# Optimization experiments

Measured on AMD Instinct MI355X. Metric: run time of the kernel, lower is better.

## Reference

```python
import jax, jax.numpy as jnp
import numpy as np

N, E, T = 10000, 160000, 1600000
D, C, H = 256, 64, 1024  # d_model, d_message/channels, 4*d_model ffn hidden


def setup_inputs() -> dict:
    key = jax.random.key(0)
    ks = jax.random.split(key, 20)
    rn = lambda k, s, sc=1.0: jax.random.normal(k, s, dtype=jnp.float32) * sc
    return {
        "x": rn(ks[0], (N, D)),
        "y": rn(ks[1], (E, D)),
        "r": rn(ks[2], (E, 3)),
        "src": jax.random.randint(ks[3], (E,), 0, N),
        "dst": jax.random.randint(ks[4], (E,), 0, N),
        "tsrc": jax.random.randint(ks[5], (T,), 0, E),
        "tdst": jax.random.randint(ks[6], (T,), 0, E),
        "W_src": rn(ks[7], (D, C), 0.05), "b_src": rn(ks[8], (C,), 0.05),
        "W_dst": rn(ks[9], (D, C), 0.05), "b_dst": rn(ks[10], (C,), 0.05),
        "W_edge": rn(ks[11], (D, C), 0.05), "b_edge": rn(ks[12], (C,), 0.05),
        "attn": rn(ks[13], (C,), 0.05),
        "W1": rn(ks[14], (C, H), 0.05), "b1": rn(ks[15], (H,), 0.05),
        "W2": rn(ks[16], (H, D), 0.05), "b2": rn(ks[17], (D,), 0.05),
    }


def reference(x, y, r, src, dst, tsrc, tdst,
              W_src, b_src, W_dst, b_dst, W_edge, b_edge,
              attn, W1, b1, W2, b2):
    # per-bond message: xij = Lin_src(x)[src] + Lin_dst(x)[dst] + Lin_edge(y)  -> (E, C)
    xij = (x @ W_src + b_src)[src] + (x @ W_dst + b_dst)[dst] + (y @ W_edge + b_edge)

    # triplet angle cosine via normalized (negated) bond vectors  -> (T,)
    rnorm = -r / jnp.linalg.norm(r, axis=1, keepdims=True)
    cos_jik = jnp.clip(jnp.sum(rnorm[tsrc] * rnorm[tdst], axis=-1), -1.0 + 1e-6, 1.0 - 1e-6)

    # Chebyshev expansion: T_n(cos) = cos(n * arccos(cos))  -> (T, C)
    n = jnp.arange(C, dtype=jnp.float32)
    z_jik = jnp.cos(n[None, :] * jnp.arccos(cos_jik)[:, None])

    # triplet feature and attention logit
    e_jik = jax.nn.silu(z_jik + xij[tsrc] + xij[tdst])          # (T, C)
    logits = e_jik @ attn                                        # (T,)

    # segment softmax over triplets grouped by destination bond (edge_softmax)
    mx = jax.ops.segment_max(logits, tdst, num_segments=E)
    ex = jnp.exp(logits - mx[tdst])
    den = jax.ops.segment_sum(ex, tdst, num_segments=E)
    a = ex / den[tdst]                                           # (T,)

    # attention-weighted scatter-sum of neighbor bond features  -> (E, C)
    ft = jax.ops.segment_sum(xij[tsrc] * a[:, None], tdst, num_segments=E)

    # feedforward: Linear -> SiLU -> Linear  -> (E, D)
    return jax.nn.silu(ft @ W1 + b1) @ W2 + b2
```

## Files before the change

kernel.cpp:

```cpp
#include <hip/hip_runtime.h>

#define N_NODES 10000
#define N_EDGES 160000
#define N_TRI   1600000
#define DM      256
#define CH      64
#define HH      1024

typedef short bf16x8 __attribute__((ext_vector_type(8)));
typedef float f32x4  __attribute__((ext_vector_type(4)));

__device__ __forceinline__ unsigned short f2bf(float f) {
  unsigned int u = __float_as_uint(f);
  u += 0x7fff + ((u >> 16) & 1);
  return (unsigned short)(u >> 16);
}

__global__ __launch_bounds__(256) void k_node_proj(
    const float* __restrict__ x, const float* __restrict__ Ws, const float* __restrict__ bs,
    const float* __restrict__ Wd, const float* __restrict__ bd,
    float* __restrict__ xs, float* __restrict__ xd) {
  __shared__ float xl[4][DM];
  int tid = threadIdx.x;
  int n0 = blockIdx.x * 4;
  for (int i = tid; i < 4 * DM; i += 256) xl[i >> 8][i & 255] = x[n0 * DM + i];
  __syncthreads();
  int c = tid & 63, g = tid >> 6;
  float as = bs[c], ad = bd[c];
  for (int d = 0; d < DM; d++) {
    float xv = xl[g][d];
    as += xv * Ws[d * CH + c];
    ad += xv * Wd[d * CH + c];
  }
  int n = n0 + g;
  xs[n * CH + c] = as;
  xd[n * CH + c] = ad;
}

__global__ __launch_bounds__(256) void k_edge_proj(
    const float* __restrict__ y, const float* __restrict__ We, const float* __restrict__ be,
    const float* __restrict__ xs, const float* __restrict__ xd,
    const int* __restrict__ src, const int* __restrict__ dst,
    float* __restrict__ xij) {
  __shared__ float yl[16][DM];
  int tid = threadIdx.x;
  int e0 = blockIdx.x * 16;
  for (int i = tid; i < 16 * DM; i += 256) yl[i >> 8][i & 255] = y[e0 * DM + i];
  __syncthreads();
  int c = tid & 63, g = tid >> 6;
  float acc[4];
#pragma unroll
  for (int s = 0; s < 4; s++) acc[s] = be[c];
  for (int d = 0; d < DM; d += 4) {
    float w0 = We[(d + 0) * CH + c];
    float w1 = We[(d + 1) * CH + c];
    float w2 = We[(d + 2) * CH + c];
    float w3 = We[(d + 3) * CH + c];
#pragma unroll
    for (int s = 0; s < 4; s++) {
      const float4 yv = *(const float4*)&yl[g * 4 + s][d];
      acc[s] += yv.x * w0 + yv.y * w1 + yv.z * w2 + yv.w * w3;
    }
  }
#pragma unroll
  for (int s = 0; s < 4; s++) {
    int e = e0 + g * 4 + s;
    xij[e * CH + c] = acc[s] + xs[src[e] * CH + c] + xd[dst[e] * CH + c];
  }
}

__global__ void k_rnorm(const float* __restrict__ r, float4* __restrict__ rn4) {
  int e = blockIdx.x * 256 + threadIdx.x;
  if (e >= N_EDGES) return;
  float a = r[e * 3 + 0], b = r[e * 3 + 1], c = r[e * 3 + 2];
  float inv = rsqrtf(a * a + b * b + c * c);
  rn4[e] = (float4){-a * inv, -b * inv, -c * inv, 0.f};
}

__global__ __launch_bounds__(256) void k_theta(
    const float4* __restrict__ rn4, const int* __restrict__ tsrc, const int* __restrict__ tdst,
    float* __restrict__ theta) {
  int t = blockIdx.x * 256 + threadIdx.x;
  if (t >= N_TRI) return;
  float4 a = rn4[tsrc[t]];
  float4 b = rn4[tdst[t]];
  float c = a.x * b.x + a.y * b.y + a.z * b.z;
  c = fminf(fmaxf(c, -1.0f + 1e-6f), 1.0f - 1e-6f);
  theta[t] = acosf(c);
}

__global__ void k_hist(const int* __restrict__ tdst, int* __restrict__ cnt) {
  int t = blockIdx.x * 256 + threadIdx.x;
  if (t < N_TRI) atomicAdd(&cnt[tdst[t]], 1);
}

__global__ __launch_bounds__(256) void k_scan_sum(const int* __restrict__ cnt,
                                                  int* __restrict__ bsum, int n) {
  __shared__ int s[256];
  int b = blockIdx.x, tid = threadIdx.x;
  int tot = 0;
#pragma unroll
  for (int i = 0; i < 8; i++) {
    int idx = b * 2048 + i * 256 + tid;
    if (idx < n) tot += cnt[idx];
  }
  s[tid] = tot;
  __syncthreads();
  for (int off = 128; off > 0; off >>= 1) {
    if (tid < off) s[tid] += s[tid + off];
    __syncthreads();
  }
  if (tid == 0) bsum[b] = s[0];
}

__global__ void k_scan_top(int* __restrict__ bsum, int nb, int* __restrict__ start_last) {
  if (threadIdx.x == 0) {
    int run = 0;
    for (int i = 0; i < nb; i++) {
      int v = bsum[i];
      bsum[i] = run;
      run += v;
    }
    *start_last = run;
  }
}

__global__ __launch_bounds__(256) void k_scan_apply(const int* __restrict__ cnt,
                                                    const int* __restrict__ bsum,
                                                    int* __restrict__ start,
                                                    int* __restrict__ cur, int n) {
  __shared__ int s[256];
  int b = blockIdx.x, tid = threadIdx.x;
  int base = b * 2048 + tid * 8;
  int loc[8];
  int tot = 0;
#pragma unroll
  for (int i = 0; i < 8; i++) {
    int idx = base + i;
    int v = (idx < n) ? cnt[idx] : 0;
    loc[i] = tot;
    tot += v;
  }
  s[tid] = tot;
  __syncthreads();
  for (int off = 1; off < 256; off <<= 1) {
    int t2 = 0;
    if (tid >= off) t2 = s[tid - off];
    __syncthreads();
    if (tid >= off) s[tid] += t2;
    __syncthreads();
  }
  int excl = s[tid] - tot + bsum[b];
#pragma unroll
  for (int i = 0; i < 8; i++) {
    int idx = base + i;
    if (idx < n) {
      int v = excl + loc[i];
      start[idx] = v;
      cur[idx] = v;
    }
  }
}

__global__ void k_scatter(const int* __restrict__ tdst, int* __restrict__ cur,
                          int* __restrict__ sorted) {
  int t = blockIdx.x * 256 + threadIdx.x;
  if (t < N_TRI) {
    int p = atomicAdd(&cur[tdst[t]], 1);
    sorted[p] = t;
  }
}

__global__ __launch_bounds__(256) void k_attn_ft(
    const int* __restrict__ start, const int* __restrict__ sorted,
    const float* __restrict__ theta, const int* __restrict__ tsrc,
    const float* __restrict__ xij, const float* __restrict__ attn,
    unsigned short* __restrict__ ft) {
  int tid = threadIdx.x;
  int e = blockIdx.x * 4 + (tid >> 6);
  int lane = tid & 63;
  float lanef = (float)lane;
  int beg = start[e], end = start[e + 1];
  int deg = end - beg;
  float xd = xij[e * CH + lane];
  float av = attn[lane];
  float m = -1e30f, den = 0.f, acc = 0.f;
  if (deg > 0 && deg <= 64) {
    int ts_ = 0;
    float th_ = 0.f;
    if (lane < deg) {
      int t = sorted[beg + lane];
      ts_ = tsrc[t];
      th_ = theta[t];
    }
    int ts_cur = __shfl(ts_, 0);
    float th_cur = __shfl(th_, 0);
    float xs_cur = xij[ts_cur * CH + lane];
    for (int i = 0; i < deg; i++) {
      float th_nxt = 0.f, xs_nxt = 0.f;
      if (i + 1 < deg) {
        int ts_nxt = __shfl(ts_, i + 1);
        th_nxt = __shfl(th_, i + 1);
        xs_nxt = xij[ts_nxt * CH + lane];
      }
      float v = __cosf(th_cur * lanef) + xs_cur + xd;
      float sv = v / (1.f + __expf(-v));
      float contrib = sv * av;
#pragma unroll
      for (int off = 32; off; off >>= 1) contrib += __shfl_xor(contrib, off);
      float mn = fmaxf(m, contrib);
      float scale = __expf(m - mn);
      float p = __expf(contrib - mn);
      den = den * scale + p;
      acc = acc * scale + p * xs_cur;
      m = mn;
      th_cur = th_nxt;
      xs_cur = xs_nxt;
    }
  } else if (deg > 64) {
    for (int i = 0; i < deg; i++) {
      int t = sorted[beg + i];
      int ts = tsrc[t];
      float th = theta[t];
      float xs = xij[ts * CH + lane];
      float v = __cosf(th * lanef) + xs + xd;
      float sv = v / (1.f + __expf(-v));
      float contrib = sv * av;
#pragma unroll
      for (int off = 32; off; off >>= 1) contrib += __shfl_xor(contrib, off);
      float mn = fmaxf(m, contrib);
      float scale = __expf(m - mn);
      float p = __expf(contrib - mn);
      den = den * scale + p;
      acc = acc * scale + p * xs;
      m = mn;
    }
  }
  ft[e * CH + lane] = f2bf(deg > 0 ? acc / den : 0.f);
}

__global__ __launch_bounds__(256) void k_prep_w1p(const float* __restrict__ W1,
                                                  unsigned short* __restrict__ W1P) {
  int idx = blockIdx.x * 256 + threadIdx.x;
  int k = idx & 63, row = idx >> 6;
  int i = row & 15, t = (row >> 4) & 1, hb = row >> 5;
  int hidden = hb * 32 + ((i >> 2) << 3) + (t << 2) + (i & 3);
  W1P[idx] = f2bf(W1[k * HH + hidden]);
}

__global__ __launch_bounds__(256) void k_prep_w2t(const float* __restrict__ W2,
                                                  unsigned short* __restrict__ W2T) {
  int idx = blockIdx.x * 256 + threadIdx.x;
  int n = idx >> 10, k = idx & 1023;
  W2T[idx] = f2bf(W2[k * DM + n]);
}

__global__ __launch_bounds__(256, 3) void k_ffn_mfma3(
    const unsigned short* __restrict__ ft, const unsigned short* __restrict__ W1P,
    const float* __restrict__ b1, const unsigned short* __restrict__ W2T,
    const float* __restrict__ b2, float* __restrict__ out) {
  __shared__ __align__(16) unsigned short hbuf[2][4 * 64 * 8];
  int tid = threadIdx.x;
  int w = tid >> 6, lane = tid & 63;
  int l16 = lane & 15, q = lane >> 4;
  int e0 = blockIdx.x * 64;

  bf16x8 ftf[2];
#pragma unroll
  for (int s = 0; s < 2; s++)
    ftf[s] = *(const bf16x8*)&ft[(size_t)(e0 + w * 16 + l16) * CH + s * 32 + q * 8];

  f32x4 acc[4][4];
#pragma unroll
  for (int mt = 0; mt < 4; mt++)
#pragma unroll
    for (int nt = 0; nt < 4; nt++) acc[mt][nt] = (f32x4){0.f, 0.f, 0.f, 0.f};

  bf16x8 w1f[2][2];
#pragma unroll
  for (int t = 0; t < 2; t++)
#pragma unroll
    for (int s = 0; s < 2; s++)
      w1f[t][s] = *(const bf16x8*)&W1P[(size_t)(t * 16 + l16) * 64 + s * 32 + q * 8];

  int p = 0;
  for (int hb = 0; hb < 32; hb++) {
    bf16x8 bw[4];
#pragma unroll
    for (int nt = 0; nt < 4; nt++)
      bw[nt] = *(const bf16x8*)&W2T[(size_t)(w * 64 + nt * 16 + l16) * HH + hb * 32 + q * 8];

    f32x4 h0 = (f32x4){0.f, 0.f, 0.f, 0.f};
    f32x4 h1 = (f32x4){0.f, 0.f, 0.f, 0.f};
    h0 = __builtin_amdgcn_mfma_f32_16x16x32_bf16(w1f[0][0], ftf[0], h0, 0, 0, 0);
    h0 = __builtin_amdgcn_mfma_f32_16x16x32_bf16(w1f[0][1], ftf[1], h0, 0, 0, 0);
    h1 = __builtin_amdgcn_mfma_f32_16x16x32_bf16(w1f[1][0], ftf[0], h1, 0, 0, 0);
    h1 = __builtin_amdgcn_mfma_f32_16x16x32_bf16(w1f[1][1], ftf[1], h1, 0, 0, 0);

    const float4 bv0 = *(const float4*)&b1[hb * 32 + q * 8];
    const float4 bv1 = *(const float4*)&b1[hb * 32 + q * 8 + 4];
    float v0 = h0[0] + bv0.x, v1 = h0[1] + bv0.y, v2 = h0[2] + bv0.z, v3 = h0[3] + bv0.w;
    float w0 = h1[0] + bv1.x, w1_ = h1[1] + bv1.y, w2 = h1[2] + bv1.z, w3 = h1[3] + bv1.w;
    float s0 = v0 / (1.f + __expf(-v0)), s1 = v1 / (1.f + __expf(-v1));
    float s2 = v2 / (1.f + __expf(-v2)), s3 = v3 / (1.f + __expf(-v3));
    float t0 = w0 / (1.f + __expf(-w0)), t1 = w1_ / (1.f + __expf(-w1_));
    float t2 = w2 / (1.f + __expf(-w2)), t3 = w3 / (1.f + __expf(-w3));
    union { bf16x8 v; unsigned int u[4]; } pa;
    pa.u[0] = ((unsigned int)f2bf(s1) << 16) | f2bf(s0);
    pa.u[1] = ((unsigned int)f2bf(s3) << 16) | f2bf(s2);
    pa.u[2] = ((unsigned int)f2bf(t1) << 16) | f2bf(t0);
    pa.u[3] = ((unsigned int)f2bf(t3) << 16) | f2bf(t2);
    *(bf16x8*)&hbuf[p][(w * 64 + lane) * 8] = pa.v;

    int hbn = (hb < 31) ? hb + 1 : 31;
    bf16x8 w1n[2][2];
#pragma unroll
    for (int t = 0; t < 2; t++)
#pragma unroll
      for (int s = 0; s < 2; s++)
        w1n[t][s] = *(const bf16x8*)&W1P[(size_t)((hbn * 2 + t) * 16 + l16) * 64 + s * 32 + q * 8];

    __syncthreads();

    bf16x8 pam[4];
#pragma unroll
    for (int mt = 0; mt < 4; mt++)
      pam[mt] = *(const bf16x8*)&hbuf[p][(mt * 64 + lane) * 8];
#pragma unroll
    for (int nt = 0; nt < 4; nt++)
#pragma unroll
      for (int mt = 0; mt < 4; mt++)
        acc[mt][nt] = __builtin_amdgcn_mfma_f32_16x16x32_bf16(pam[mt], bw[nt], acc[mt][nt], 0, 0, 0);

#pragma unroll
    for (int t = 0; t < 2; t++)
#pragma unroll
      for (int s = 0; s < 2; s++) w1f[t][s] = w1n[t][s];
    p ^= 1;
  }

#pragma unroll
  for (int nt = 0; nt < 4; nt++) {
    int col = w * 64 + nt * 16 + l16;
    float b2v = b2[col];
#pragma unroll
    for (int mt = 0; mt < 4; mt++) {
      int erow = e0 + mt * 16 + q * 4;
#pragma unroll
      for (int r = 0; r < 4; r++)
        out[(size_t)(erow + r) * DM + col] = acc[mt][nt][r] + b2v;
    }
  }
}

extern "C" void kernel_launch(void* const* d_in, const int* in_sizes, int n_in,
                              void* d_out, int out_size, void* d_ws, size_t ws_size,
                              hipStream_t stream) {
  (void)in_sizes; (void)n_in; (void)out_size; (void)ws_size;
  const float* x      = (const float*)d_in[0];
  const float* y      = (const float*)d_in[1];
  const float* r      = (const float*)d_in[2];
  const int*   src    = (const int*)d_in[3];
  const int*   dst    = (const int*)d_in[4];
  const int*   tsrc   = (const int*)d_in[5];
  const int*   tdst   = (const int*)d_in[6];
  const float* W_src  = (const float*)d_in[7];
  const float* b_src  = (const float*)d_in[8];
  const float* W_dst  = (const float*)d_in[9];
  const float* b_dst  = (const float*)d_in[10];
  const float* W_edge = (const float*)d_in[11];
  const float* b_edge = (const float*)d_in[12];
  const float* attn   = (const float*)d_in[13];
  const float* W1     = (const float*)d_in[14];
  const float* b1     = (const float*)d_in[15];
  const float* W2     = (const float*)d_in[16];
  const float* b2     = (const float*)d_in[17];
  float* out = (float*)d_out;

  char* wsp = (char*)d_ws;
  auto alloc = [&](size_t bytes) -> char* {
    char* p = wsp;
    wsp += (bytes + 255) & ~(size_t)255;
    return p;
  };
  float* xs     = (float*)alloc((size_t)N_NODES * CH * 4);
  float* xd     = (float*)alloc((size_t)N_NODES * CH * 4);
  float* xij    = (float*)alloc((size_t)N_EDGES * CH * 4);
  float4* rn4   = (float4*)alloc((size_t)N_EDGES * 16);
  float* theta  = (float*)alloc((size_t)N_TRI * 4);
  int*   cnt    = (int*)alloc((size_t)N_EDGES * 4);
  int*   start  = (int*)alloc((size_t)(N_EDGES + 1) * 4);
  int*   cur    = (int*)alloc((size_t)N_EDGES * 4);
  int*   bsum   = (int*)alloc(1024 * 4);
  int*   sorted = (int*)alloc((size_t)N_TRI * 4);
  unsigned short* ftb = (unsigned short*)alloc((size_t)N_EDGES * CH * 2);
  unsigned short* W1P = (unsigned short*)alloc((size_t)CH * HH * 2);
  unsigned short* W2T = (unsigned short*)alloc((size_t)HH * DM * 2);

  const int NB = (N_EDGES + 2047) / 2048;

  k_prep_w1p<<<(CH * HH) / 256, 256, 0, stream>>>(W1, W1P);
  k_prep_w2t<<<(HH * DM) / 256, 256, 0, stream>>>(W2, W2T);

  k_node_proj<<<N_NODES / 4, 256, 0, stream>>>(x, W_src, b_src, W_dst, b_dst, xs, xd);
  k_rnorm<<<N_EDGES / 256, 256, 0, stream>>>(r, rn4);
  k_edge_proj<<<N_EDGES / 16, 256, 0, stream>>>(y, W_edge, b_edge, xs, xd, src, dst, xij);
  k_theta<<<N_TRI / 256, 256, 0, stream>>>(rn4, tsrc, tdst, theta);

  hipMemsetAsync(cnt, 0, (size_t)N_EDGES * 4, stream);
  k_hist<<<N_TRI / 256, 256, 0, stream>>>(tdst, cnt);
  k_scan_sum<<<NB, 256, 0, stream>>>(cnt, bsum, N_EDGES);
  k_scan_top<<<1, 64, 0, stream>>>(bsum, NB, &start[N_EDGES]);
  k_scan_apply<<<NB, 256, 0, stream>>>(cnt, bsum, start, cur, N_EDGES);
  k_scatter<<<N_TRI / 256, 256, 0, stream>>>(tdst, cur, sorted);

  k_attn_ft<<<N_EDGES / 4, 256, 0, stream>>>(start, sorted, theta, tsrc, xij, attn, ftb);
  k_ffn_mfma3<<<N_EDGES / 64, 256, 0, stream>>>(ftb, W1P, b1, W2T, b2, out);
}
```

Baseline: 1.228 ms.

## Use two-pass lane-parallel softmax and remove LDS exchange in FFN kernel

In the attention kernel, degrees up to 64 now take a two-pass path. The first pass collects each triplet's logit into one lane, then a wave reduction computes the max and denominator. A second pass reloads neighbour features and accumulates the attention-weighted sum, replacing the per-step online-softmax rescaling with its serial exps. In the FFN kernel, each wave now computes the hidden activations for all four row tiles itself and feeds them straight into the second MFMA, removing the shared-memory buffer and block barrier. The cost is redundant first-layer MFMA work, more registers and lower launch-bound occupancy, plus a second gather of xij in attention.

```diff
diff --git a/kernel.cpp b/kernel.cpp
--- a/kernel.cpp
+++ b/kernel.cpp
@@ -184,7 +184,7 @@
   int deg = end - beg;
   float xd = xij[e * CH + lane];
   float av = attn[lane];
-  float m = -1e30f, den = 0.f, acc = 0.f;
+  float acc = 0.f;
   if (deg > 0 && deg <= 64) {
     int ts_ = 0;
     float th_ = 0.f;
@@ -193,6 +193,7 @@
       ts_ = tsrc[t];
       th_ = theta[t];
     }
+    float l_mine = -1e30f;
     int ts_cur = __shfl(ts_, 0);
     float th_cur = __shfl(th_, 0);
     float xs_cur = xij[ts_cur * CH + lane];
@@ -208,16 +209,31 @@
       float contrib = sv * av;
 #pragma unroll
       for (int off = 32; off; off >>= 1) contrib += __shfl_xor(contrib, off);
-      float mn = fmaxf(m, contrib);
-      float scale = __expf(m - mn);
-      float p = __expf(contrib - mn);
-      den = den * scale + p;
-      acc = acc * scale + p * xs_cur;
-      m = mn;
+      if (lane == i) l_mine = contrib;
       th_cur = th_nxt;
       xs_cur = xs_nxt;
     }
+    float mx = l_mine;
+#pragma unroll
+    for (int off = 32; off; off >>= 1) mx = fmaxf(mx, __shfl_xor(mx, off));
+    float ex = (lane < deg) ? __expf(l_mine - mx) : 0.f;
+    float den = ex;
+#pragma unroll
+    for (int off = 32; off; off >>= 1) den += __shfl_xor(den, off);
+    float a_mine = ex / den;
+    ts_cur = __shfl(ts_, 0);
+    xs_cur = xij[ts_cur * CH + lane];
+    for (int i = 0; i < deg; i++) {
+      float xs_nxt = 0.f;
+      if (i + 1 < deg) {
+        int ts_nxt = __shfl(ts_, i + 1);
+        xs_nxt = xij[ts_nxt * CH + lane];
+      }
+      acc += __shfl(a_mine, i) * xs_cur;
+      xs_cur = xs_nxt;
+    }
   } else if (deg > 64) {
+    float m = -1e30f, den = 0.f;
     for (int i = 0; i < deg; i++) {
       int t = sorted[beg + i];
       int ts = tsrc[t];
@@ -235,8 +251,9 @@
       acc = acc * scale + p * xs;
       m = mn;
     }
-  }
-  ft[e * CH + lane] = f2bf(deg > 0 ? acc / den : 0.f);
+    acc = acc / den;
+  }
+  ft[e * CH + lane] = f2bf(acc);
 }
 
 __global__ __launch_bounds__(256) void k_prep_w1p(const float* __restrict__ W1,
@@ -255,20 +272,21 @@
   W2T[idx] = f2bf(W2[k * DM + n]);
 }
 
-__global__ __launch_bounds__(256, 3) void k_ffn_mfma3(
+__global__ __launch_bounds__(256, 2) void k_ffn_mfma4(
     const unsigned short* __restrict__ ft, const unsigned short* __restrict__ W1P,
     const float* __restrict__ b1, const unsigned short* __restrict__ W2T,
     const float* __restrict__ b2, float* __restrict__ out) {
-  __shared__ __align__(16) unsigned short hbuf[2][4 * 64 * 8];
   int tid = threadIdx.x;
   int w = tid >> 6, lane = tid & 63;
   int l16 = lane & 15, q = lane >> 4;
   int e0 = blockIdx.x * 64;
 
-  bf16x8 ftf[2];
-#pragma unroll
-  for (int s = 0; s < 2; s++)
-    ftf[s] = *(const bf16x8*)&ft[(size_t)(e0 + w * 16 + l16) * CH + s * 32 + q * 8];
+  bf16x8 ftf[4][2];
+#pragma unroll
+  for (int mt = 0; mt < 4; mt++)
+#pragma unroll
+    for (int s = 0; s < 2; s++)
+      ftf[mt][s] = *(const bf16x8*)&ft[(size_t)(e0 + mt * 16 + l16) * CH + s * 32 + q * 8];
 
   f32x4 acc[4][4];
 #pragma unroll
@@ -283,60 +301,53 @@
     for (int s = 0; s < 2; s++)
       w1f[t][s] = *(const bf16x8*)&W1P[(size_t)(t * 16 + l16) * 64 + s * 32 + q * 8];
 
-  int p = 0;
   for (int hb = 0; hb < 32; hb++) {
     bf16x8 bw[4];
 #pragma unroll
     for (int nt = 0; nt < 4; nt++)
       bw[nt] = *(const bf16x8*)&W2T[(size_t)(w * 64 + nt * 16 + l16) * HH + hb * 32 + q * 8];
 
-    f32x4 h0 = (f32x4){0.f, 0.f, 0.f, 0.f};
-    f32x4 h1 = (f32x4){0.f, 0.f, 0.f, 0.f};
-    h0 = __builtin_amdgcn_mfma_f32_16x16x32_bf16(w1f[0][0], ftf[0], h0, 0, 0, 0);
-    h0 = __builtin_amdgcn_mfma_f32_16x16x32_bf16(w1f[0][1], ftf[1], h0, 0, 0, 0);
-    h1 = __builtin_amdgcn_mfma_f32_16x16x32_bf16(w1f[1][0], ftf[0], h1, 0, 0, 0);
-    h1 = __builtin_amdgcn_mfma_f32_16x16x32_bf16(w1f[1][1], ftf[1], h1, 0, 0, 0);
+    int hbn = (hb < 31) ? hb + 1 : 31;
+    bf16x8 w1n[2][2];
+#pragma unroll
+    for (int t = 0; t < 2; t++)
+#pragma unroll
+      for (int s = 0; s < 2; s++)
+        w1n[t][s] = *(const bf16x8*)&W1P[(size_t)((hbn * 2 + t) * 16 + l16) * 64 + s * 32 + q * 8];
 
     const float4 bv0 = *(const float4*)&b1[hb * 32 + q * 8];
     const float4 bv1 = *(const float4*)&b1[hb * 32 + q * 8 + 4];
-    float v0 = h0[0] + bv0.x, v1 = h0[1] + bv0.y, v2 = h0[2] + bv0.z, v3 = h0[3] + bv0.w;
-    float w0 = h1[0] + bv1.x, w1_ = h1[1] + bv1.y, w2 = h1[2] + bv1.z, w3 = h1[3] + bv1.w;
-    float s0 = v0 / (1.f + __expf(-v0)), s1 = v1 / (1.f + __expf(-v1));
-    float s2 = v2 / (1.f + __expf(-v2)), s3 = v3 / (1.f + __expf(-v3));
-    float t0 = w0 / (1.f + __expf(-w0)), t1 = w1_ / (1.f + __expf(-w1_));
-    float t2 = w2 / (1.f + __expf(-w2)), t3 = w3 / (1.f + __expf(-w3));
-    union { bf16x8 v; unsigned int u[4]; } pa;
-    pa.u[0] = ((unsigned int)f2bf(s1) << 16) | f2bf(s0);
-    pa.u[1] = ((unsigned int)f2bf(s3) << 16) | f2bf(s2);
-    pa.u[2] = ((unsigned int)f2bf(t1) << 16) | f2bf(t0);
-    pa.u[3] = ((unsigned int)f2bf(t3) << 16) | f2bf(t2);
-    *(bf16x8*)&hbuf[p][(w * 64 + lane) * 8] = pa.v;
-
-    int hbn = (hb < 31) ? hb + 1 : 31;
-    bf16x8 w1n[2][2];
+
+#pragma unroll
+    for (int mt = 0; mt < 4; mt++) {
+      f32x4 h0 = (f32x4){0.f, 0.f, 0.f, 0.f};
+      f32x4 h1 = (f32x4){0.f, 0.f, 0.f, 0.f};
+      h0 = __builtin_amdgcn_mfma_f32_16x16x32_bf16(w1f[0][0], ftf[mt][0], h0, 0, 0, 0);
+      h0 = __builtin_amdgcn_mfma_f32_16x16x32_bf16(w1f[0][1], ftf[mt][1], h0, 0, 0, 0);
+      h1 = __builtin_amdgcn_mfma_f32_16x16x32_bf16(w1f[1][0], ftf[mt][0], h1, 0, 0, 0);
+      h1 = __builtin_amdgcn_mfma_f32_16x16x32_bf16(w1f[1][1], ftf[mt][1], h1, 0, 0, 0);
+
+      float v0 = h0[0] + bv0.x, v1 = h0[1] + bv0.y, v2 = h0[2] + bv0.z, v3 = h0[3] + bv0.w;
+      float u0 = h1[0] + bv1.x, u1 = h1[1] + bv1.y, u2 = h1[2] + bv1.z, u3 = h1[3] + bv1.w;
+      float s0 = v0 / (1.f + __expf(-v0)), s1 = v1 / (1.f + __expf(-v1));
+      float s2 = v2 / (1.f + __expf(-v2)), s3 = v3 / (1.f + __expf(-v3));
+      float t0 = u0 / (1.f + __expf(-u0)), t1 = u1 / (1.f + __expf(-u1));
+      float t2 = u2 / (1.f + __expf(-u2)), t3 = u3 / (1.f + __expf(-u3));
+      union { bf16x8 v; unsigned int u[4]; } pa;
+      pa.u[0] = ((unsigned int)f2bf(s1) << 16) | f2bf(s0);
+      pa.u[1] = ((unsigned int)f2bf(s3) << 16) | f2bf(s2);
+      pa.u[2] = ((unsigned int)f2bf(t1) << 16) | f2bf(t0);
+      pa.u[3] = ((unsigned int)f2bf(t3) << 16) | f2bf(t2);
+
+#pragma unroll
+      for (int nt = 0; nt < 4; nt++)
+        acc[mt][nt] = __builtin_amdgcn_mfma_f32_16x16x32_bf16(pa.v, bw[nt], acc[mt][nt], 0, 0, 0);
+    }
+
 #pragma unroll
     for (int t = 0; t < 2; t++)
 #pragma unroll
-      for (int s = 0; s < 2; s++)
-        w1n[t][s] = *(const bf16x8*)&W1P[(size_t)((hbn * 2 + t) * 16 + l16) * 64 + s * 32 + q * 8];
-
-    __syncthreads();
-
-    bf16x8 pam[4];
-#pragma unroll
-    for (int mt = 0; mt < 4; mt++)
-      pam[mt] = *(const bf16x8*)&hbuf[p][(mt * 64 + lane) * 8];
-#pragma unroll
-    for (int nt = 0; nt < 4; nt++)
-#pragma unroll
-      for (int mt = 0; mt < 4; mt++)
-        acc[mt][nt] = __builtin_amdgcn_mfma_f32_16x16x32_bf16(pam[mt], bw[nt], acc[mt][nt], 0, 0, 0);
-
-#pragma unroll
-    for (int t = 0; t < 2; t++)
-#pragma unroll
       for (int s = 0; s < 2; s++) w1f[t][s] = w1n[t][s];
-    p ^= 1;
   }
 
 #pragma unroll
@@ -415,5 +426,5 @@
   k_scatter<<<N_TRI / 256, 256, 0, stream>>>(tdst, cur, sorted);
 
   k_attn_ft<<<N_EDGES / 4, 256, 0, stream>>>(start, sorted, theta, tsrc, xij, attn, ftb);
-  k_ffn_mfma3<<<N_EDGES / 64, 256, 0, stream>>>(ftb, W1P, b1, W2T, b2, out);
-}
+  k_ffn_mfma4<<<N_EDGES / 64, 256, 0, stream>>>(ftb, W1P, b1, W2T, b2, out);
+}
```

Measured after the change: 1.433 ms. 1.17x slower.
